# Optimization experiments

Measured on AMD Instinct MI355X. Metric: run time of the kernel, lower is better.

Reference implementation:

```python
import jax, jax.numpy as jnp
import numpy as np

N = 50000          # nodes
E = 1_600_000      # edges (avg degree 32)
F_IN, H1, H2 = 512, 128, 64


def setup_inputs() -> dict:
    key = jax.random.key(0)
    ks = jax.random.split(key, 9)
    x = jax.random.normal(ks[0], (N, F_IN), jnp.float32)
    edge_index = jax.random.randint(ks[1], (2, E), 0, N, jnp.int32)
    # Glorot-ish scaled weights
    W1 = jax.random.normal(ks[2], (F_IN, H1), jnp.float32) / np.sqrt(F_IN)
    b1 = jnp.zeros((H1,), jnp.float32)
    W2 = jax.random.normal(ks[3], (H1, H2), jnp.float32) / np.sqrt(H1)
    b2 = jnp.zeros((H2,), jnp.float32)
    W3 = jax.random.normal(ks[4], (H1, H2), jnp.float32) / np.sqrt(H1)
    b3 = jnp.zeros((H2,), jnp.float32)
    eps = jax.random.normal(ks[5], (N, H2), jnp.float32)
    return {"x": x, "edge_index": edge_index, "W1": W1, "b1": b1,
            "W2": W2, "b2": b2, "W3": W3, "b3": b3, "eps": eps}


def _gcn_norm(edge_index, n, dtype):
    # add self loops, then symmetric normalization deg^-1/2 A_hat deg^-1/2
    loop = jnp.arange(n, dtype=edge_index.dtype)
    src = jnp.concatenate([edge_index[0], loop])
    dst = jnp.concatenate([edge_index[1], loop])
    deg = jax.ops.segment_sum(jnp.ones_like(dst, dtype=dtype), dst, num_segments=n)
    dinv = jax.lax.rsqrt(jnp.maximum(deg, 1.0))
    norm = dinv[src] * dinv[dst]          # [E + N]
    return src, dst, norm


def _gcn_conv(h, src, dst, norm, W, b):
    hw = h @ W                             # dense linear transform [N, out]
    msg = hw[src] * norm[:, None]          # gather + scale      [E+N, out]
    return jax.ops.segment_sum(msg, dst, num_segments=h.shape[0]) + b


def reference(x, edge_index, W1, b1, W2, b2, W3, b3, eps):
    src, dst, norm = _gcn_norm(edge_index, x.shape[0], x.dtype)
    h1 = _gcn_conv(x, src, dst, norm, W1, b1)      # gc1
    mu = _gcn_conv(h1, src, dst, norm, W2, b2)     # gc2
    logvar = _gcn_conv(h1, src, dst, norm, W3, b3) # gc3
    # faithful to source: std = exp(logvar), z = eps*std + mu (training path)
    z = eps * jnp.exp(logvar) + mu
    return z
```

## Files before the change

kernel.cpp:

```cpp
#include <hip/hip_runtime.h>
#include <math.h>

#define NN   50000
#define NE   1600000
#define FIN  512
#define H1F  128
#define NBUK  391
#define BIN_EPB 4096
#define NBIN  391

typedef __attribute__((ext_vector_type(8))) short bf16x8;
typedef __attribute__((ext_vector_type(4))) float f32x4;
typedef __attribute__((ext_vector_type(2))) float f32x2;

__device__ __forceinline__ float bflo(unsigned v) { return __uint_as_float(v << 16); }
__device__ __forceinline__ float bfhi(unsigned v) { return __uint_as_float(v & 0xffff0000u); }
__device__ __forceinline__ unsigned short f2bf(float f) {
  unsigned u = __float_as_uint(f);
  u += 0x7fffu + ((u >> 16) & 1u);
  return (unsigned short)(u >> 16);
}
__device__ __forceinline__ unsigned pack2bf(float a, float b) {
  return (unsigned)f2bf(a) | ((unsigned)f2bf(b) << 16);
}

#if defined(__has_builtin)
#  if __has_builtin(__builtin_amdgcn_cvt_pk_f32_fp8) && __has_builtin(__builtin_amdgcn_cvt_pk_fp8_f32)
#    define HW_FP8 1
#  endif
#endif
#ifndef HW_FP8
#  define HW_FP8 0
#endif

__device__ __forceinline__ float fp8dec_sw(unsigned v, int sh) {
  unsigned b = (v >> sh) & 0xffu;
  unsigned bits = ((b & 0x80u) << 24) | ((b & 0x7fu) << 20);
  return __uint_as_float(bits) * 0x1.0p+120f;
}
__device__ __forceinline__ unsigned fp8enc_sw(float f) {
  unsigned u = __float_as_uint(f * 0x1.0p-120f);
  unsigned s = (u >> 24) & 0x80u;
  u &= 0x7fffffffu;
  u += 0x7ffffu + ((u >> 20) & 1u);
  unsigned e = u >> 20;
  if (e > 0x7fu) e = 0x7fu;
  return s | e;
}

__device__ __forceinline__ void fp8dec4p(unsigned v, f32x2& lo, f32x2& hi) {
#if HW_FP8
  lo = __builtin_amdgcn_cvt_pk_f32_fp8(v, false);
  hi = __builtin_amdgcn_cvt_pk_f32_fp8(v, true);
#else
  lo = (f32x2){fp8dec_sw(v, 0), fp8dec_sw(v, 8)};
  hi = (f32x2){fp8dec_sw(v, 16), fp8dec_sw(v, 24)};
#endif
}
__device__ __forceinline__ unsigned fp8enc4(float a, float b, float c, float d) {
#if HW_FP8
  unsigned r = (unsigned)__builtin_amdgcn_cvt_pk_fp8_f32(a, b, 0, false);
  r = (unsigned)__builtin_amdgcn_cvt_pk_fp8_f32(c, d, (int)r, true);
  return r;
#else
  return fp8enc_sw(a) | (fp8enc_sw(b) << 8) | (fp8enc_sw(c) << 16) | (fp8enc_sw(d) << 24);
#endif
}


__global__ __launch_bounds__(256) void k_binhist(const int* __restrict__ ei,
                                                 int* __restrict__ gh) {
  __shared__ int hist[NBUK];
  int t  = threadIdx.x;
  int e0 = blockIdx.x * BIN_EPB;
  for (int b = t; b < NBUK; b += 256) hist[b] = 0;
  __syncthreads();
#pragma unroll
  for (int j = 0; j < 16; ++j) {
    int e = e0 + j * 256 + t;
    if (e < NE) atomicAdd(&hist[ei[NE + e] >> 7], 1);
  }
  __syncthreads();
  for (int b = t; b < NBUK; b += 256) gh[(size_t)b * NBIN + blockIdx.x] = hist[b];
}

__global__ __launch_bounds__(64) void k_rowscan(int* __restrict__ gh,
                                                int* __restrict__ btot) {
  int row  = blockIdx.x;
  int lane = threadIdx.x;
  int* g = gh + (size_t)row * NBIN;
  int carry = 0;
  for (int c = 0; c < (NBIN + 63) / 64; ++c) {
    int idx = c * 64 + lane;
    int v = (idx < NBIN) ? g[idx] : 0;
    int incl = v;
#pragma unroll
    for (int off = 1; off < 64; off <<= 1) {
      int u = __shfl_up(incl, off, 64);
      if (lane >= off) incl += u;
    }
    if (idx < NBIN) g[idx] = carry + (incl - v);
    carry += __shfl(incl, 63, 64);
  }
  if (lane == 0) btot[row] = carry;
}

__global__ __launch_bounds__(512) void k_bscan(const int* __restrict__ btot,
                                               int* __restrict__ bbase) {
  __shared__ int ts[512];
  int t = threadIdx.x;
  int v = (t < NBUK) ? btot[t] : 0;
  ts[t] = v;
  __syncthreads();
  for (int off = 1; off < 512; off <<= 1) {
    int val = ts[t];
    int add = (t >= off) ? ts[t - off] : 0;
    __syncthreads();
    ts[t] = val + add;
    __syncthreads();
  }
  if (t < NBUK) bbase[t] = ts[t] - v;
  if (t == NBUK - 1) bbase[NBUK] = ts[t];
}

__global__ __launch_bounds__(256) void k_binscat(const int* __restrict__ ei,
                                                 const int* __restrict__ gh,
                                                 const int* __restrict__ bbase,
                                                 unsigned* __restrict__ tmp) {
  __shared__ int hist[NBUK];
  __shared__ int sbase[NBUK];
  int t  = threadIdx.x;
  int e0 = blockIdx.x * BIN_EPB;
  for (int b = t; b < NBUK; b += 256) hist[b] = 0;
  __syncthreads();

  unsigned short d16[16];
  unsigned short p16[16];
#pragma unroll
  for (int j = 0; j < 16; ++j) {
    int e = e0 + j * 256 + t;
    d16[j] = 0xFFFFu;
    if (e < NE) {
      int d = ei[NE + e];
      d16[j] = (unsigned short)d;
      p16[j] = (unsigned short)atomicAdd(&hist[d >> 7], 1);
    }
  }
  __syncthreads();
  for (int b = t; b < NBUK; b += 256)
    sbase[b] = bbase[b] + gh[(size_t)b * NBIN + blockIdx.x];
  __syncthreads();
#pragma unroll
  for (int j = 0; j < 16; ++j) {
    int e = e0 + j * 256 + t;
    if (e < NE) {
      int s = ei[e];
      int d = (int)d16[j];
      tmp[sbase[d >> 7] + (int)p16[j]] = ((unsigned)s << 16) | (unsigned)d;
    }
  }
}

__global__ __launch_bounds__(256) void k_fill2x(const unsigned* __restrict__ tmp,
                                                const int* __restrict__ bbase,
                                                int* __restrict__ rowptr,
                                                float* __restrict__ dinv,
                                                int* __restrict__ csr) {
  __shared__ int cnt[128];
  __shared__ int lofs[128];
  __shared__ int cur[128];
  __shared__ int ts[256];
  int b  = blockIdx.x;
  int t  = threadIdx.x;
  int n0 = b << 7;
  int beg = bbase[b];
  int end = bbase[b + 1];
  if (t < 128) { cnt[t] = 0; cur[t] = 0; }
  __syncthreads();
  for (int i = beg + t; i < end; i += 256)
    atomicAdd(&cnt[tmp[i] & 127u], 1);
  __syncthreads();
  int v = (t < 128) ? cnt[t] : 0;
  ts[t] = v;
  __syncthreads();
  for (int off = 1; off < 128; off <<= 1) {
    int val = ts[t];
    int add = (t >= off) ? ts[t - off] : 0;
    __syncthreads();
    ts[t] = val + add;
    __syncthreads();
  }
  if (t < 128) {
    int excl = ts[t] - v;
    lofs[t] = beg + excl;
    int n = n0 + t;
    if (n < NN) {
      rowptr[n] = beg + excl;
      dinv[n]   = rsqrtf((float)(v + 1));
    }
  }
  if (b == NBUK - 1 && t == 0) rowptr[NN] = end;
  __syncthreads();
  for (int i = beg + t; i < end; i += 256) {
    unsigned pk = tmp[i];
    int dl = (int)(pk & 127u);
    int s  = (int)(pk >> 16);
    int p  = atomicAdd(&cur[dl], 1);
    csr[lofs[dl] + p] = s;
  }
}


__global__ __launch_bounds__(256) void k_cvtw1f(const float* __restrict__ W,
                                                unsigned short* __restrict__ W1f) {
  int i = blockIdx.x * 256 + threadIdx.x;
  if (i >= 16 * 8 * 64) return;
  int s = i >> 9, rem = i & 511, f = rem >> 6, lane = rem & 63;
  int row = f * 16 + (lane & 15);
  int kb  = s * 32 + (lane >> 4) * 8;
  unsigned short c8[8];
#pragma unroll
  for (int j = 0; j < 8; ++j) c8[j] = f2bf(W[(size_t)(kb + j) * H1F + row]);
  *(uint4*)&W1f[(size_t)i * 8] = *(uint4*)c8;
}

__global__ __launch_bounds__(256) void k_cvtw23f(const float* __restrict__ W2,
                                                 const float* __restrict__ W3,
                                                 unsigned short* __restrict__ Wf) {
  int i = blockIdx.x * 256 + threadIdx.x;
  if (i >= 4 * 8 * 64) return;
  int s = i >> 9, rem = i & 511, f = rem >> 6, lane = rem & 63;
  int row = f * 16 + (lane & 15);
  int kb  = s * 32 + (lane >> 4) * 8;
  int pair = row >> 5;
  const float* Wsrc = (pair & 1) ? W3 : W2;
  int c = (pair >> 1) * 32 + (row & 31);
  unsigned short c8[8];
#pragma unroll
  for (int j = 0; j < 8; ++j) c8[j] = f2bf(Wsrc[(size_t)(kb + j) * 64 + c]);
  *(uint4*)&Wf[(size_t)i * 8] = *(uint4*)c8;
}


#define G1_ABUF 5120
#define G1_BBUF 8192
#define G1_BUF  (G1_ABUF + G1_BBUF)
#define G1_NSTEP 16

__global__ __launch_bounds__(256) void k_gemm1m(const float* __restrict__ X,
                                                const uint4* __restrict__ W1fv,
                                                const float* __restrict__ dinv,
                                                unsigned* __restrict__ out8) {
  __shared__ char lds[2 * G1_BUF];
  int tid  = threadIdx.x;
  int row0 = blockIdx.x * 64;
  int w    = tid >> 6;
  int wr   = w >> 1, wc = w & 1;
  int lane = tid & 63;

  int ar = tid >> 2, aq = tid & 3;

  float4 av0, av1;
  uint4  bu0, bu1;

  auto load_g = [&](int s) {
    int k0 = s * 32;
    int row = row0 + ar;
    av0 = make_float4(0.f, 0.f, 0.f, 0.f);
    av1 = av0;
    if (row < NN) {
      const float* gp = X + (size_t)row * FIN + k0 + aq * 8;
      av0 = *(const float4*)gp;
      av1 = *(const float4*)(gp + 4);
    }
    const uint4* bp = W1fv + (size_t)s * 512;
    bu0 = bp[tid];
    bu1 = bp[tid + 256];
  };
  auto store_l = [&](int buf) {
    char* Ab = lds + buf * G1_BUF;
    char* Bb = Ab + G1_ABUF;
    uint4 ap;
    ap.x = pack2bf(av0.x, av0.y); ap.y = pack2bf(av0.z, av0.w);
    ap.z = pack2bf(av1.x, av1.y); ap.w = pack2bf(av1.z, av1.w);
    *(uint4*)(Ab + ar * 80 + aq * 16) = ap;
    *(uint4*)(Bb + tid * 16)        = bu0;
    *(uint4*)(Bb + tid * 16 + 4096) = bu1;
  };

  f32x4 acc[2][4];
#pragma unroll
  for (int u = 0; u < 2; ++u)
#pragma unroll
    for (int f = 0; f < 4; ++f) acc[u][f] = (f32x4){0.f, 0.f, 0.f, 0.f};

  load_g(0);
  store_l(0);

  for (int s = 0; s < G1_NSTEP; ++s) {
    if (s + 1 < G1_NSTEP) load_g(s + 1);
    __syncthreads();
    const char* Ab = lds + (s & 1) * G1_BUF;
    const char* Bb = Ab + G1_ABUF;
    bf16x8 xa0 = *(const bf16x8*)(Ab + (wr * 32 + (lane & 15)) * 80 + (lane >> 4) * 16);
    bf16x8 xa1 = *(const bf16x8*)(Ab + (wr * 32 + 16 + (lane & 15)) * 80 + (lane >> 4) * 16);
#pragma unroll
    for (int f = 0; f < 4; ++f) {
      bf16x8 bt = *(const bf16x8*)(Bb + (wc * 4 + f) * 1024 + lane * 16);
      acc[0][f] = __builtin_amdgcn_mfma_f32_16x16x32_bf16(bt, xa0, acc[0][f], 0, 0, 0);
      acc[1][f] = __builtin_amdgcn_mfma_f32_16x16x32_bf16(bt, xa1, acc[1][f], 0, 0, 0);
    }
    if (s + 1 < G1_NSTEP) store_l((s + 1) & 1);
  }

#pragma unroll
  for (int u = 0; u < 2; ++u) {
    int orow = row0 + wr * 32 + u * 16 + (lane & 15);
    if (orow < NN) {
      float di = dinv[orow];
      size_t base = (size_t)orow * 32;
#pragma unroll
      for (int f = 0; f < 4; ++f) {
        int col = (wc * 4 + f) * 16 + (lane >> 4) * 4;
        out8[base + (col >> 2)] = fp8enc4(di * acc[u][f][0], di * acc[u][f][1],
                                          di * acc[u][f][2], di * acc[u][f][3]);
      }
    }
  }
}


template<bool BIAS, bool OUTBF>
__global__ __launch_bounds__(256) void k_agg8(const unsigned* __restrict__ feat,
                                              const int* __restrict__ rowptr,
                                              const int* __restrict__ csr,
                                              const float* __restrict__ dinv,
                                              const float* __restrict__ bias,
                                              void* __restrict__ out) {
  int gw   = (blockIdx.x * 256 + threadIdx.x) >> 5;
  int lane = threadIdx.x & 31;
  if (gw >= NN) return;
  int beg = rowptr[gw], end = rowptr[gw + 1];
  float di = dinv[gw];
  f32x2 aA = (f32x2){0.f, 0.f}, bA = (f32x2){0.f, 0.f};
  f32x2 aB = (f32x2){0.f, 0.f}, bB = (f32x2){0.f, 0.f};

  for (int e = beg; e < end; e += 32) {
    int cnt = end - e; if (cnt > 32) cnt = 32;
    int sv = 0;
    if (lane < cnt) sv = csr[e + lane];
    int j = 0;
    for (; j + 8 <= cnt; j += 8) {
      unsigned vv[8];
#pragma unroll
      for (int q = 0; q < 8; ++q) {
        int s = __shfl(sv, j + q, 32);
        vv[q] = feat[(size_t)s * 32 + lane];
      }
#pragma unroll
      for (int q = 0; q < 8; ++q) {
        f32x2 lo, hi;
        fp8dec4p(vv[q], lo, hi);
        if (q & 1) { aB += lo; bB += hi; }
        else       { aA += lo; bA += hi; }
      }
    }
    for (; j < cnt; ++j) {
      int s = __shfl(sv, j, 32);
      f32x2 lo, hi;
      fp8dec4p(feat[(size_t)s * 32 + lane], lo, hi);
      aA += lo; bA += hi;
    }
  }
  {
    f32x2 lo, hi;
    fp8dec4p(feat[(size_t)gw * 32 + lane], lo, hi);
    aA += lo; bA += hi;
  }
  f32x2 s01 = aA + aB;
  f32x2 s23 = bA + bB;
  float a0 = di * s01[0], a1 = di * s01[1];
  float a2 = di * s23[0], a3 = di * s23[1];
  if (BIAS) {
    float4 bb = *(const float4*)&bias[lane * 4];
    a0 += bb.x; a1 += bb.y; a2 += bb.z; a3 += bb.w;
  }
  if (OUTBF) {
    uint2 pk; pk.x = pack2bf(a0, a1); pk.y = pack2bf(a2, a3);
    *(uint2*)&((unsigned*)out)[(size_t)gw * 64 + lane * 2] = pk;
  } else {
    ((unsigned*)out)[(size_t)gw * 32 + lane] = fp8enc4(di * a0, di * a1, di * a2, di * a3);
  }
}


#define G2_ASTRIDE 272
#define G2_AOFF    (64 * G2_ASTRIDE)
#define G2_BBYTES  32768

__global__ __launch_bounds__(256) void k_gemm2m(const unsigned short* __restrict__ Gb,
                                                const uint4* __restrict__ W23fv,
                                                const float* __restrict__ b2,
                                                const float* __restrict__ b3,
                                                const float* __restrict__ eps,
                                                float* __restrict__ z) {
  __shared__ char lds[G2_AOFF + G2_BBYTES];
  int tid  = threadIdx.x;
  int row0 = blockIdx.x * 64;
  int w    = tid >> 6;
  int wr   = w >> 1, wc = w & 1;
  int lane = tid & 63;

  {
    int ar = tid >> 2, aq = tid & 3;
    int row = row0 + ar;
    uint4 a0 = {}, a1 = {}, a2 = {}, a3 = {};
    if (row < NN) {
      const uint4* gp = (const uint4*)(Gb + (size_t)row * H1F) + aq * 4;
      a0 = gp[0]; a1 = gp[1]; a2 = gp[2]; a3 = gp[3];
    }
    char* Ab = lds + ar * G2_ASTRIDE + aq * 64;
    *(uint4*)(Ab)      = a0;
    *(uint4*)(Ab + 16) = a1;
    *(uint4*)(Ab + 32) = a2;
    *(uint4*)(Ab + 48) = a3;
  }
  {
    uint4* Bb = (uint4*)(lds + G2_AOFF);
#pragma unroll
    for (int j = 0; j < 8; ++j) Bb[tid + j * 256] = W23fv[tid + j * 256];
  }
  __syncthreads();

  f32x4 acc[2][4];
#pragma unroll
  for (int u = 0; u < 2; ++u)
#pragma unroll
    for (int f = 0; f < 4; ++f) acc[u][f] = (f32x4){0.f, 0.f, 0.f, 0.f};

#pragma unroll
  for (int s = 0; s < 4; ++s) {
    bf16x8 xa0 = *(const bf16x8*)(lds + (wr * 32 + (lane & 15)) * G2_ASTRIDE + s * 64 + (lane >> 4) * 16);
    bf16x8 xa1 = *(const bf16x8*)(lds + (wr * 32 + 16 + (lane & 15)) * G2_ASTRIDE + s * 64 + (lane >> 4) * 16);
#pragma unroll
    for (int f = 0; f < 4; ++f) {
      bf16x8 bt = *(const bf16x8*)(lds + G2_AOFF + ((s * 512 + (wc * 4 + f) * 64 + lane) << 4));
      acc[0][f] = __builtin_amdgcn_mfma_f32_16x16x32_bf16(bt, xa0, acc[0][f], 0, 0, 0);
      acc[1][f] = __builtin_amdgcn_mfma_f32_16x16x32_bf16(bt, xa1, acc[1][f], 0, 0, 0);
    }
  }

  int q = lane >> 4;
#pragma unroll
  for (int u = 0; u < 2; ++u) {
    int orow = row0 + wr * 32 + u * 16 + (lane & 15);
    if (orow < NN) {
      size_t base = (size_t)orow * 64;
#pragma unroll
      for (int f2 = 0; f2 < 2; ++f2) {
        int c = wc * 32 + f2 * 16 + q * 4;
        float4 ev = *(const float4*)&eps[base + c];
        f32x4 mu = acc[u][f2];
        f32x4 lv = acc[u][f2 + 2];
        float4 zo;
        zo.x = ev.x * __expf(lv[0] + b3[c + 0]) + mu[0] + b2[c + 0];
        zo.y = ev.y * __expf(lv[1] + b3[c + 1]) + mu[1] + b2[c + 1];
        zo.z = ev.z * __expf(lv[2] + b3[c + 2]) + mu[2] + b2[c + 2];
        zo.w = ev.w * __expf(lv[3] + b3[c + 3]) + mu[3] + b2[c + 3];
        *(float4*)&z[base + c] = zo;
      }
    }
  }
}


extern "C" void kernel_launch(void* const* d_in, const int* in_sizes, int n_in,
                              void* d_out, int out_size, void* d_ws, size_t ws_size,
                              hipStream_t stream) {
  const float* x   = (const float*)d_in[0];
  const int*   ei  = (const int*)  d_in[1];
  const float* W1  = (const float*)d_in[2];
  const float* b1  = (const float*)d_in[3];
  const float* W2  = (const float*)d_in[4];
  const float* b2  = (const float*)d_in[5];
  const float* W3  = (const float*)d_in[6];
  const float* b3  = (const float*)d_in[7];
  const float* eps = (const float*)d_in[8];
  float* z = (float*)d_out;

  char* ws = (char*)d_ws;
  size_t o = 0;
  auto alloc = [&](size_t bytes) -> void* {
    void* p = ws + o;
    o = (o + bytes + 255) & ~(size_t)255;
    return p;
  };
  int*   gh     = (int*)  alloc((size_t)NBUK * NBIN * 4);
  int*   btot   = (int*)  alloc((size_t)NBUK * 4);
  int*   bbase  = (int*)  alloc((size_t)(NBUK + 1) * 4);
  int*   rowptr = (int*)  alloc((size_t)(NN + 1) * 4);
  float* dinv   = (float*)alloc((size_t)NN * 4);
  int*   csr    = (int*)  alloc((size_t)NE * 4);
  unsigned* tmp = (unsigned*)alloc((size_t)NE * 4);
  unsigned short* W1f  = (unsigned short*)alloc((size_t)16 * 8 * 64 * 8 * 2);
  unsigned short* W23f = (unsigned short*)alloc((size_t)4 * 8 * 64 * 8 * 2);
  unsigned* hw8 = (unsigned*)alloc((size_t)NN * 32 * 4);
  unsigned* h8  = (unsigned*)alloc((size_t)NN * 32 * 4);
  unsigned short* gb = (unsigned short*)alloc((size_t)NN * H1F * 2);

  k_binhist<<<NBIN, 256, 0, stream>>>(ei, gh);
  k_rowscan<<<NBUK, 64, 0, stream>>>(gh, btot);
  k_bscan  <<<1, 512, 0, stream>>>(btot, bbase);
  k_binscat<<<NBIN, 256, 0, stream>>>(ei, gh, bbase, tmp);
  k_fill2x <<<NBUK, 256, 0, stream>>>(tmp, bbase, rowptr, dinv, csr);
  k_cvtw1f <<<32, 256, 0, stream>>>(W1, W1f);
  k_cvtw23f<<<8, 256, 0, stream>>>(W2, W3, W23f);

  k_gemm1m <<<(NN + 63) / 64, 256, 0, stream>>>(x, (const uint4*)W1f, dinv, hw8);
  k_agg8<true,  false><<<(NN * 32 + 255) / 256, 256, 0, stream>>>(hw8, rowptr, csr, dinv, b1, (void*)h8);
  k_agg8<false, true ><<<(NN * 32 + 255) / 256, 256, 0, stream>>>(h8,  rowptr, csr, dinv, nullptr, (void*)gb);
  k_gemm2m <<<(NN + 63) / 64, 256, 0, stream>>>(gb, (const uint4*)W23f, b2, b3, eps, z);
}
```

Baseline: 142.9 us.

## Map each node to a full 64-lane wavefront with four edge subgroups in aggregation

```diff
diff --git a/kernel.cpp b/kernel.cpp
--- a/kernel.cpp
+++ b/kernel.cpp
@@ -337,59 +337,81 @@
                                               const float* __restrict__ dinv,
                                               const float* __restrict__ bias,
                                               void* __restrict__ out) {
-  int gw   = (blockIdx.x * 256 + threadIdx.x) >> 5;
-  int lane = threadIdx.x & 31;
+  int gw   = (blockIdx.x * 256 + threadIdx.x) >> 6;
+  int lane = threadIdx.x & 63;
   if (gw >= NN) return;
+  int g  = lane >> 4;
+  int sl = lane & 15;
   int beg = rowptr[gw], end = rowptr[gw + 1];
   float di = dinv[gw];
-  f32x2 aA = (f32x2){0.f, 0.f}, bA = (f32x2){0.f, 0.f};
-  f32x2 aB = (f32x2){0.f, 0.f}, bB = (f32x2){0.f, 0.f};
-
-  for (int e = beg; e < end; e += 32) {
-    int cnt = end - e; if (cnt > 32) cnt = 32;
+  f32x2 acc0 = (f32x2){0.f, 0.f}, acc1 = (f32x2){0.f, 0.f};
+  f32x2 acc2 = (f32x2){0.f, 0.f}, acc3 = (f32x2){0.f, 0.f};
+
+  for (int e = beg; e < end; e += 64) {
+    int cnt = end - e; if (cnt > 64) cnt = 64;
     int sv = 0;
     if (lane < cnt) sv = csr[e + lane];
     int j = 0;
     for (; j + 8 <= cnt; j += 8) {
-      unsigned vv[8];
-#pragma unroll
-      for (int q = 0; q < 8; ++q) {
-        int s = __shfl(sv, j + q, 32);
-        vv[q] = feat[(size_t)s * 32 + lane];
+      int s0 = __shfl(sv, j + g, 64);
+      int s1 = __shfl(sv, j + 4 + g, 64);
+      uint2 v0 = *(const uint2*)&feat[(size_t)s0 * 32 + sl * 2];
+      uint2 v1 = *(const uint2*)&feat[(size_t)s1 * 32 + sl * 2];
+      f32x2 lo, hi;
+      fp8dec4p(v0.x, lo, hi); acc0 += lo; acc1 += hi;
+      fp8dec4p(v0.y, lo, hi); acc2 += lo; acc3 += hi;
+      fp8dec4p(v1.x, lo, hi); acc0 += lo; acc1 += hi;
+      fp8dec4p(v1.y, lo, hi); acc2 += lo; acc3 += hi;
+    }
+    for (; j < cnt; j += 4) {
+      int idx  = j + g;
+      int srcl = (idx < cnt) ? idx : 0;
+      int s = __shfl(sv, srcl, 64);
+      if (idx < cnt) {
+        uint2 v = *(const uint2*)&feat[(size_t)s * 32 + sl * 2];
+        f32x2 lo, hi;
+        fp8dec4p(v.x, lo, hi); acc0 += lo; acc1 += hi;
+        fp8dec4p(v.y, lo, hi); acc2 += lo; acc3 += hi;
       }
-#pragma unroll
-      for (int q = 0; q < 8; ++q) {
-        f32x2 lo, hi;
-        fp8dec4p(vv[q], lo, hi);
-        if (q & 1) { aB += lo; bB += hi; }
-        else       { aA += lo; bA += hi; }
-      }
-    }
-    for (; j < cnt; ++j) {
-      int s = __shfl(sv, j, 32);
-      f32x2 lo, hi;
-      fp8dec4p(feat[(size_t)s * 32 + lane], lo, hi);
-      aA += lo; bA += hi;
-    }
-  }
-  {
+    }
+  }
+  if (g == 0) {
+    uint2 v = *(const uint2*)&feat[(size_t)gw * 32 + sl * 2];
     f32x2 lo, hi;
-    fp8dec4p(feat[(size_t)gw * 32 + lane], lo, hi);
-    aA += lo; bA += hi;
-  }
-  f32x2 s01 = aA + aB;
-  f32x2 s23 = bA + bB;
-  float a0 = di * s01[0], a1 = di * s01[1];
-  float a2 = di * s23[0], a3 = di * s23[1];
+    fp8dec4p(v.x, lo, hi); acc0 += lo; acc1 += hi;
+    fp8dec4p(v.y, lo, hi); acc2 += lo; acc3 += hi;
+  }
+#pragma unroll
+  for (int d = 16; d <= 32; d <<= 1) {
+    f32x2 t0, t1, t2, t3;
+    t0[0] = __shfl_xor(acc0[0], d, 64); t0[1] = __shfl_xor(acc0[1], d, 64);
+    t1[0] = __shfl_xor(acc1[0], d, 64); t1[1] = __shfl_xor(acc1[1], d, 64);
+    t2[0] = __shfl_xor(acc2[0], d, 64); t2[1] = __shfl_xor(acc2[1], d, 64);
+    t3[0] = __shfl_xor(acc3[0], d, 64); t3[1] = __shfl_xor(acc3[1], d, 64);
+    acc0 += t0; acc1 += t1; acc2 += t2; acc3 += t3;
+  }
+  float a0 = di * acc0[0], a1 = di * acc0[1];
+  float a2 = di * acc1[0], a3 = di * acc1[1];
+  float a4 = di * acc2[0], a5 = di * acc2[1];
+  float a6 = di * acc3[0], a7 = di * acc3[1];
   if (BIAS) {
-    float4 bb = *(const float4*)&bias[lane * 4];
-    a0 += bb.x; a1 += bb.y; a2 += bb.z; a3 += bb.w;
-  }
-  if (OUTBF) {
-    uint2 pk; pk.x = pack2bf(a0, a1); pk.y = pack2bf(a2, a3);
-    *(uint2*)&((unsigned*)out)[(size_t)gw * 64 + lane * 2] = pk;
-  } else {
-    ((unsigned*)out)[(size_t)gw * 32 + lane] = fp8enc4(di * a0, di * a1, di * a2, di * a3);
+    float4 b0 = *(const float4*)&bias[sl * 8];
+    float4 b1v = *(const float4*)&bias[sl * 8 + 4];
+    a0 += b0.x; a1 += b0.y; a2 += b0.z; a3 += b0.w;
+    a4 += b1v.x; a5 += b1v.y; a6 += b1v.z; a7 += b1v.w;
+  }
+  if (g == 0) {
+    if (OUTBF) {
+      uint4 pk;
+      pk.x = pack2bf(a0, a1); pk.y = pack2bf(a2, a3);
+      pk.z = pack2bf(a4, a5); pk.w = pack2bf(a6, a7);
+      *(uint4*)&((unsigned*)out)[(size_t)gw * 64 + sl * 4] = pk;
+    } else {
+      uint2 pk;
+      pk.x = fp8enc4(di * a0, di * a1, di * a2, di * a3);
+      pk.y = fp8enc4(di * a4, di * a5, di * a6, di * a7);
+      *(uint2*)&((unsigned*)out)[(size_t)gw * 32 + sl * 2] = pk;
+    }
   }
 }
 
@@ -517,7 +539,7 @@
   k_cvtw23f<<<8, 256, 0, stream>>>(W2, W3, W23f);
 
   k_gemm1m <<<(NN + 63) / 64, 256, 0, stream>>>(x, (const uint4*)W1f, dinv, hw8);
-  k_agg8<true,  false><<<(NN * 32 + 255) / 256, 256, 0, stream>>>(hw8, rowptr, csr, dinv, b1, (void*)h8);
-  k_agg8<false, true ><<<(NN * 32 + 255) / 256, 256, 0, stream>>>(h8,  rowptr, csr, dinv, nullptr, (void*)gb);
+  k_agg8<true,  false><<<(NN * 64 + 255) / 256, 256, 0, stream>>>(hw8, rowptr, csr, dinv, b1, (void*)h8);
+  k_agg8<false, true ><<<(NN * 64 + 255) / 256, 256, 0, stream>>>(h8,  rowptr, csr, dinv, nullptr, (void*)gb);
   k_gemm2m <<<(NN + 63) / 64, 256, 0, stream>>>(gb, (const uint4*)W23f, b2, b3, eps, z);
 }
```

After: 146.9 us. +2.8%, slower.
